# Kernel optimization log

Hardware: AMD Instinct MI355X
Metric: run time of the kernel (lower is better)

## Reference

```python
import jax, jax.numpy as jnp
import numpy as np

IN_CH, OUT_CH, IN_W, K, PAD = 64, 64, 2048, 3, 1
OUT_W = IN_W + 2 * PAD - K + 1  # 2048


def setup_inputs() -> dict:
    key = jax.random.key(0)
    k1, k2, k3 = jax.random.split(key, 3)
    x = jax.random.normal(k1, (32, IN_CH, IN_W), dtype=jnp.float32)
    weights = jax.random.normal(k2, (OUT_W, OUT_CH, IN_CH, K), dtype=jnp.float32)
    bias = jax.random.normal(k3, (OUT_CH, OUT_W), dtype=jnp.float32)
    return {"x": x, "weights": weights, "bias": bias}


def reference(x, weights, bias):
    # x: (B, IC, W); weights: (OW, OC, IC, K); bias: (OC, OW)
    xp = jnp.pad(x, ((0, 0), (0, 0), (PAD, PAD)))  # (B, IC, W+2p)
    # Gather sliding windows: patches[b, ic, w, k] = xp[b, ic, w + k]
    idx = jnp.arange(OUT_W)[:, None] + jnp.arange(K)[None, :]  # (OW, K)
    patches = xp[:, :, idx]  # (B, IC, OW, K)
    # Per-position unshared contraction over (ic, k)
    out = jnp.einsum('bcwk,wock->bow', patches, weights)  # (B, OC, OW)
    return out + bias[None, :, :]
```

## Files before the change

kernel.cpp:

```cpp
#include <hip/hip_runtime.h>
#include <hip/hip_bf16.h>

typedef _Float16 f16x4 __attribute__((ext_vector_type(4)));
typedef _Float16 f16x8 __attribute__((ext_vector_type(8)));
typedef float f32x4 __attribute__((ext_vector_type(4)));

#define IN_CH   64
#define OUT_CH  64
#define W_TOT   2048
#define KW      3
#define B_TOT   32
#define CK      192
#define LDSTRIDE 200

__global__ __launch_bounds__(256, 4)
void lc1d_kernel(const float* __restrict__ x,
                 const float* __restrict__ wts,
                 const float* __restrict__ bias,
                 float* __restrict__ out) {
    __shared__ _Float16 Wt[OUT_CH * LDSTRIDE];
    __shared__ _Float16 Xp[B_TOT * LDSTRIDE];

    const int tid = threadIdx.x;
    const int bid = blockIdx.x;
    const int w = (bid & 7) * 256 + (bid >> 3);

    const float* wsrc = wts + (size_t)w * (OUT_CH * CK);
    #pragma unroll
    for (int i = 0; i < 12; ++i) {
        int e = i * 1024 + tid * 4;
        float4 v = *reinterpret_cast<const float4*>(wsrc + e);
        int r = e / CK;
        int c = e - r * CK;
        f16x4 h = { (_Float16)v.x, (_Float16)v.y, (_Float16)v.z, (_Float16)v.w };
        *reinterpret_cast<f16x4*>(&Wt[r * LDSTRIDE + c]) = h;
    }

    #pragma unroll
    for (int j = 0; j < 8; ++j) {
        int p = tid + 256 * j;
        int b = p >> 6;
        int c = p & 63;
        const float* row = x + (size_t)p * W_TOT;
        #pragma unroll
        for (int k = 0; k < KW; ++k) {
            int v = w - 1 + k;
            float xv = (v >= 0 && v < W_TOT) ? row[v] : 0.0f;
            Xp[b * LDSTRIDE + c * 3 + k] = (_Float16)xv;
        }
    }

    __syncthreads();

    const int lane = tid & 63;
    const int wv   = tid >> 6;
    const int l15  = lane & 15;
    const int kg   = lane >> 4;

    const _Float16* Xb = &Xp[l15 * LDSTRIDE + kg * 8];
    const _Float16* Wb = &Wt[(wv * 16 + l15) * LDSTRIDE + kg * 8];

    f32x4 acc0 = {0.f, 0.f, 0.f, 0.f};
    f32x4 acc1 = {0.f, 0.f, 0.f, 0.f};
    #pragma unroll
    for (int kk = 0; kk < 6; ++kk) {
        f16x8 a0 = *reinterpret_cast<const f16x8*>(Xb + kk * 32);
        f16x8 a1 = *reinterpret_cast<const f16x8*>(Xb + 16 * LDSTRIDE + kk * 32);
        f16x8 bf = *reinterpret_cast<const f16x8*>(Wb + kk * 32);
        acc0 = __builtin_amdgcn_mfma_f32_16x16x32_f16(a0, bf, acc0, 0, 0, 0);
        acc1 = __builtin_amdgcn_mfma_f32_16x16x32_f16(a1, bf, acc1, 0, 0, 0);
    }

    const int o = wv * 16 + l15;
    const float bv = bias[o * W_TOT + w];
    #pragma unroll
    for (int r = 0; r < 4; ++r) {
        int b0 = kg * 4 + r;
        out[((size_t)(b0 * OUT_CH + o)) * W_TOT + w] = acc0[r] + bv;
        int b1 = 16 + kg * 4 + r;
        out[((size_t)(b1 * OUT_CH + o)) * W_TOT + w] = acc1[r] + bv;
    }
}

extern "C" void kernel_launch(void* const* d_in, const int* in_sizes, int n_in,
                              void* d_out, int out_size, void* d_ws, size_t ws_size,
                              hipStream_t stream) {
    const float* x    = (const float*)d_in[0];
    const float* wts  = (const float*)d_in[1];
    const float* bias = (const float*)d_in[2];
    float* out = (float*)d_out;
    hipLaunchKernelGGL(lc1d_kernel, dim3(2048), dim3(256), 0, stream,
                       x, wts, bias, out);
}
```

Baseline: 219.3 us.

## Load weight fragments directly into registers and batch x window loads

Weights are now read from global memory straight into the per-lane MFMA B-fragment registers, dropping the shared-memory weight tile and its round trip. The x window loads are issued as float2 vector loads into registers before any LDS stores, so all global loads are in flight together. Removing the weight tile shrinks LDS use, and the occupancy hint goes from 4 to 5 blocks. In exchange, each lane's global weight reads are 32-byte chunks at a 768-byte stride rather than fully coalesced float4 rows, and register pressure rises.

```diff
diff --git a/kernel.cpp b/kernel.cpp
--- a/kernel.cpp
+++ b/kernel.cpp
@@ -1,7 +1,5 @@
 #include <hip/hip_runtime.h>
-#include <hip/hip_bf16.h>
 
-typedef _Float16 f16x4 __attribute__((ext_vector_type(4)));
 typedef _Float16 f16x8 __attribute__((ext_vector_type(8)));
 typedef float f32x4 __attribute__((ext_vector_type(4)));
 
@@ -11,68 +9,91 @@
 #define KW      3
 #define B_TOT   32
 #define CK      192
-#define LDSTRIDE 200
+#define LDST    200
 
-__global__ __launch_bounds__(256, 4)
+static __device__ __forceinline__ f16x8 cvt8(const float4& a, const float4& b) {
+    f16x8 r;
+    r[0] = (_Float16)a.x; r[1] = (_Float16)a.y; r[2] = (_Float16)a.z; r[3] = (_Float16)a.w;
+    r[4] = (_Float16)b.x; r[5] = (_Float16)b.y; r[6] = (_Float16)b.z; r[7] = (_Float16)b.w;
+    return r;
+}
+
+__global__ __launch_bounds__(256, 5)
 void lc1d_kernel(const float* __restrict__ x,
                  const float* __restrict__ wts,
                  const float* __restrict__ bias,
                  float* __restrict__ out) {
-    __shared__ _Float16 Wt[OUT_CH * LDSTRIDE];
-    __shared__ _Float16 Xp[B_TOT * LDSTRIDE];
+    __shared__ _Float16 Xp[B_TOT * LDST];
 
     const int tid = threadIdx.x;
     const int bid = blockIdx.x;
     const int w = (bid & 7) * 256 + (bid >> 3);
 
-    const float* wsrc = wts + (size_t)w * (OUT_CH * CK);
+    const int lane = tid & 63;
+    const int wv   = tid >> 6;
+    const int l15  = lane & 15;
+    const int kg   = lane >> 4;
+
+    float xv[8][3];
     #pragma unroll
-    for (int i = 0; i < 12; ++i) {
-        int e = i * 1024 + tid * 4;
-        float4 v = *reinterpret_cast<const float4*>(wsrc + e);
-        int r = e / CK;
-        int c = e - r * CK;
-        f16x4 h = { (_Float16)v.x, (_Float16)v.y, (_Float16)v.z, (_Float16)v.w };
-        *reinterpret_cast<f16x4*>(&Wt[r * LDSTRIDE + c]) = h;
+    for (int j = 0; j < 8; ++j) {
+        const float* row = x + (size_t)(tid + 256 * j) * W_TOT;
+        if (w == 0) {
+            float2 lo = *reinterpret_cast<const float2*>(row);
+            xv[j][0] = 0.f;  xv[j][1] = lo.x; xv[j][2] = lo.y;
+        } else if (w == W_TOT - 1) {
+            float2 lo = *reinterpret_cast<const float2*>(row + W_TOT - 2);
+            xv[j][0] = lo.x; xv[j][1] = lo.y; xv[j][2] = 0.f;
+        } else if ((w - 1) & 1) {
+            float2 lo = *reinterpret_cast<const float2*>(row + (w - 1 - 1));
+            float2 hi = *reinterpret_cast<const float2*>(row + (w - 1 + 1));
+            xv[j][0] = lo.y; xv[j][1] = hi.x; xv[j][2] = hi.y;
+        } else {
+            float2 lo = *reinterpret_cast<const float2*>(row + (w - 1));
+            float2 hi = *reinterpret_cast<const float2*>(row + (w + 1));
+            xv[j][0] = lo.x; xv[j][1] = lo.y; xv[j][2] = hi.x;
+        }
     }
+
+    const int o = wv * 16 + l15;
+    const float* wsrc = wts + (size_t)w * (OUT_CH * CK) + o * CK + kg * 8;
+    float4 wf[6][2];
+    #pragma unroll
+    for (int ks = 0; ks < 6; ++ks) {
+        wf[ks][0] = *reinterpret_cast<const float4*>(wsrc + ks * 32);
+        wf[ks][1] = *reinterpret_cast<const float4*>(wsrc + ks * 32 + 4);
+    }
+
+    const float bv = bias[o * W_TOT + w];
 
     #pragma unroll
     for (int j = 0; j < 8; ++j) {
         int p = tid + 256 * j;
         int b = p >> 6;
         int c = p & 63;
-        const float* row = x + (size_t)p * W_TOT;
-        #pragma unroll
-        for (int k = 0; k < KW; ++k) {
-            int v = w - 1 + k;
-            float xv = (v >= 0 && v < W_TOT) ? row[v] : 0.0f;
-            Xp[b * LDSTRIDE + c * 3 + k] = (_Float16)xv;
-        }
+        _Float16* dst = &Xp[b * LDST + c * 3];
+        dst[0] = (_Float16)xv[j][0];
+        dst[1] = (_Float16)xv[j][1];
+        dst[2] = (_Float16)xv[j][2];
     }
+
+    f16x8 bw[6];
+    #pragma unroll
+    for (int ks = 0; ks < 6; ++ks) bw[ks] = cvt8(wf[ks][0], wf[ks][1]);
 
     __syncthreads();
 
-    const int lane = tid & 63;
-    const int wv   = tid >> 6;
-    const int l15  = lane & 15;
-    const int kg   = lane >> 4;
-
-    const _Float16* Xb = &Xp[l15 * LDSTRIDE + kg * 8];
-    const _Float16* Wb = &Wt[(wv * 16 + l15) * LDSTRIDE + kg * 8];
-
+    const _Float16* Xb = &Xp[l15 * LDST + kg * 8];
     f32x4 acc0 = {0.f, 0.f, 0.f, 0.f};
     f32x4 acc1 = {0.f, 0.f, 0.f, 0.f};
     #pragma unroll
-    for (int kk = 0; kk < 6; ++kk) {
-        f16x8 a0 = *reinterpret_cast<const f16x8*>(Xb + kk * 32);
-        f16x8 a1 = *reinterpret_cast<const f16x8*>(Xb + 16 * LDSTRIDE + kk * 32);
-        f16x8 bf = *reinterpret_cast<const f16x8*>(Wb + kk * 32);
-        acc0 = __builtin_amdgcn_mfma_f32_16x16x32_f16(a0, bf, acc0, 0, 0, 0);
-        acc1 = __builtin_amdgcn_mfma_f32_16x16x32_f16(a1, bf, acc1, 0, 0, 0);
+    for (int ks = 0; ks < 6; ++ks) {
+        f16x8 a0 = *reinterpret_cast<const f16x8*>(Xb + ks * 32);
+        f16x8 a1 = *reinterpret_cast<const f16x8*>(Xb + 16 * LDST + ks * 32);
+        acc0 = __builtin_amdgcn_mfma_f32_16x16x32_f16(a0, bw[ks], acc0, 0, 0, 0);
+        acc1 = __builtin_amdgcn_mfma_f32_16x16x32_f16(a1, bw[ks], acc1, 0, 0, 0);
     }
 
-    const int o = wv * 16 + l15;
-    const float bv = bias[o * W_TOT + w];
     #pragma unroll
     for (int r = 0; r < 4; ++r) {
         int b0 = kg * 4 + r;
```

New measurement: 207.7 us. 5.3% less time.

## Process four output positions per block with double-buffered weight prefetch

Applied to the files above, without the earlier changes.

Each block now handles four consecutive output positions instead of one. Weights for the next position are prefetched into registers and written into a double-buffered LDS tile while the current position's MFMAs run. The input window is loaded once as six contiguous values per row instead of three scattered scalar loads per position. Outputs and bias are written and read as float4 vectors. This cuts redundant x loads, uncoalesced stores and per-block setup. In exchange there are four times fewer blocks, more registers per thread and extra barriers.

```diff
diff --git a/kernel.cpp b/kernel.cpp
--- a/kernel.cpp
+++ b/kernel.cpp
@@ -1,85 +1,144 @@
 #include <hip/hip_runtime.h>
-#include <hip/hip_bf16.h>
+#include <stdint.h>
 
-typedef _Float16 f16x4 __attribute__((ext_vector_type(4)));
 typedef _Float16 f16x8 __attribute__((ext_vector_type(8)));
+typedef _Float16 f16x4v __attribute__((ext_vector_type(4)));
 typedef float f32x4 __attribute__((ext_vector_type(4)));
 
-#define IN_CH   64
-#define OUT_CH  64
-#define W_TOT   2048
-#define KW      3
-#define B_TOT   32
-#define CK      192
-#define LDSTRIDE 200
+#define W_TOT  2048
+#define CK     192
+#define NW     4
+#define WROWST 200
+#define XPST   200
 
-__global__ __launch_bounds__(256, 4)
+__global__ __launch_bounds__(256, 2)
 void lc1d_kernel(const float* __restrict__ x,
                  const float* __restrict__ wts,
                  const float* __restrict__ bias,
                  float* __restrict__ out) {
-    __shared__ _Float16 Wt[OUT_CH * LDSTRIDE];
-    __shared__ _Float16 Xp[B_TOT * LDSTRIDE];
+    __shared__ _Float16 Wb[2][64 * WROWST];
+    __shared__ _Float16 Xp[32 * XPST];
 
-    const int tid = threadIdx.x;
-    const int bid = blockIdx.x;
-    const int w = (bid & 7) * 256 + (bid >> 3);
-
-    const float* wsrc = wts + (size_t)w * (OUT_CH * CK);
-    #pragma unroll
-    for (int i = 0; i < 12; ++i) {
-        int e = i * 1024 + tid * 4;
-        float4 v = *reinterpret_cast<const float4*>(wsrc + e);
-        int r = e / CK;
-        int c = e - r * CK;
-        f16x4 h = { (_Float16)v.x, (_Float16)v.y, (_Float16)v.z, (_Float16)v.w };
-        *reinterpret_cast<f16x4*>(&Wt[r * LDSTRIDE + c]) = h;
-    }
-
-    #pragma unroll
-    for (int j = 0; j < 8; ++j) {
-        int p = tid + 256 * j;
-        int b = p >> 6;
-        int c = p & 63;
-        const float* row = x + (size_t)p * W_TOT;
-        #pragma unroll
-        for (int k = 0; k < KW; ++k) {
-            int v = w - 1 + k;
-            float xv = (v >= 0 && v < W_TOT) ? row[v] : 0.0f;
-            Xp[b * LDSTRIDE + c * 3 + k] = (_Float16)xv;
-        }
-    }
-
-    __syncthreads();
+    const int tid  = threadIdx.x;
+    const int bid  = blockIdx.x;
+    const int w0   = ((bid & 7) * 64 + (bid >> 3)) * NW;
 
     const int lane = tid & 63;
     const int wv   = tid >> 6;
     const int l15  = lane & 15;
     const int kg   = lane >> 4;
+    const int o    = wv * 16 + l15;
 
-    const _Float16* Xb = &Xp[l15 * LDSTRIDE + kg * 8];
-    const _Float16* Wb = &Wt[(wv * 16 + l15) * LDSTRIDE + kg * 8];
-
-    f32x4 acc0 = {0.f, 0.f, 0.f, 0.f};
-    f32x4 acc1 = {0.f, 0.f, 0.f, 0.f};
+    float xw[8][6];
     #pragma unroll
-    for (int kk = 0; kk < 6; ++kk) {
-        f16x8 a0 = *reinterpret_cast<const f16x8*>(Xb + kk * 32);
-        f16x8 a1 = *reinterpret_cast<const f16x8*>(Xb + 16 * LDSTRIDE + kk * 32);
-        f16x8 bf = *reinterpret_cast<const f16x8*>(Wb + kk * 32);
-        acc0 = __builtin_amdgcn_mfma_f32_16x16x32_f16(a0, bf, acc0, 0, 0, 0);
-        acc1 = __builtin_amdgcn_mfma_f32_16x16x32_f16(a1, bf, acc1, 0, 0, 0);
+    for (int j = 0; j < 8; ++j) {
+        const float* row = x + (size_t)(tid + 256 * j) * W_TOT;
+        if (w0 == 0) {
+            float2 a = *(const float2*)(row + 0);
+            float2 b = *(const float2*)(row + 2);
+            float2 c = *(const float2*)(row + 4);
+            xw[j][0] = 0.f;  xw[j][1] = a.x; xw[j][2] = a.y;
+            xw[j][3] = b.x;  xw[j][4] = b.y; xw[j][5] = c.x;
+        } else if (w0 == W_TOT - NW) {
+            float2 a = *(const float2*)(row + W_TOT - 6);
+            float2 b = *(const float2*)(row + W_TOT - 4);
+            float2 c = *(const float2*)(row + W_TOT - 2);
+            xw[j][0] = a.y; xw[j][1] = b.x; xw[j][2] = b.y;
+            xw[j][3] = c.x; xw[j][4] = c.y; xw[j][5] = 0.f;
+        } else {
+            float2 a = *(const float2*)(row + w0 - 2);
+            float2 b = *(const float2*)(row + w0);
+            float2 c = *(const float2*)(row + w0 + 2);
+            float2 d = *(const float2*)(row + w0 + 4);
+            xw[j][0] = a.y; xw[j][1] = b.x; xw[j][2] = b.y;
+            xw[j][3] = c.x; xw[j][4] = c.y; xw[j][5] = d.x;
+        }
     }
 
-    const int o = wv * 16 + l15;
-    const float bv = bias[o * W_TOT + w];
+    f32x4 wr[12];
+    {
+        const float* wp = wts + (size_t)w0 * (64 * CK);
+        #pragma unroll
+        for (int t = 0; t < 12; ++t)
+            wr[t] = *(const f32x4*)(wp + t * 1024 + tid * 4);
+    }
+    const f32x4 bv = *(const f32x4*)(bias + (size_t)o * W_TOT + w0);
+
+    _Float16 xh[8][6];
     #pragma unroll
-    for (int r = 0; r < 4; ++r) {
-        int b0 = kg * 4 + r;
-        out[((size_t)(b0 * OUT_CH + o)) * W_TOT + w] = acc0[r] + bv;
-        int b1 = 16 + kg * 4 + r;
-        out[((size_t)(b1 * OUT_CH + o)) * W_TOT + w] = acc1[r] + bv;
+    for (int j = 0; j < 8; ++j)
+        #pragma unroll
+        for (int s = 0; s < 6; ++s) xh[j][s] = (_Float16)xw[j][s];
+
+    #pragma unroll
+    for (int t = 0; t < 12; ++t) {
+        int e = t * 1024 + tid * 4;
+        int r = e / 192, c = e % 192;
+        f16x4v h = { (_Float16)wr[t][0], (_Float16)wr[t][1],
+                     (_Float16)wr[t][2], (_Float16)wr[t][3] };
+        *(f16x4v*)(&Wb[0][r * WROWST + c]) = h;
     }
+    #pragma unroll
+    for (int j = 0; j < 8; ++j) {
+        int p = tid + 256 * j;
+        _Float16* dst = &Xp[(p >> 6) * XPST + (p & 63) * 3];
+        dst[0] = xh[j][0]; dst[1] = xh[j][1]; dst[2] = xh[j][2];
+    }
+    __syncthreads();
+
+    f32x4 acc[NW][2];
+    #pragma unroll
+    for (int i = 0; i < NW; ++i) { acc[i][0] = {0.f,0.f,0.f,0.f}; acc[i][1] = {0.f,0.f,0.f,0.f}; }
+
+    const _Float16* Xb = &Xp[l15 * XPST + kg * 8];
+
+    #pragma unroll
+    for (int i = 0; i < NW; ++i) {
+        if (i < NW - 1) {
+            const float* wp = wts + (size_t)(w0 + i + 1) * (64 * CK);
+            #pragma unroll
+            for (int t = 0; t < 12; ++t)
+                wr[t] = *(const f32x4*)(wp + t * 1024 + tid * 4);
+        }
+        const _Float16* Wcur = &Wb[i & 1][o * WROWST + kg * 8];
+        #pragma unroll
+        for (int ks = 0; ks < 6; ++ks) {
+            f16x8 a0 = *(const f16x8*)(Xb + ks * 32);
+            f16x8 a1 = *(const f16x8*)(Xb + 16 * XPST + ks * 32);
+            f16x8 bw = *(const f16x8*)(Wcur + ks * 32);
+            acc[i][0] = __builtin_amdgcn_mfma_f32_16x16x32_f16(a0, bw, acc[i][0], 0, 0, 0);
+            acc[i][1] = __builtin_amdgcn_mfma_f32_16x16x32_f16(a1, bw, acc[i][1], 0, 0, 0);
+        }
+        __syncthreads();
+        if (i < NW - 1) {
+            _Float16* Wnxt = &Wb[(i + 1) & 1][0];
+            #pragma unroll
+            for (int t = 0; t < 12; ++t) {
+                int e = t * 1024 + tid * 4;
+                int r = e / 192, c = e % 192;
+                f16x4v h = { (_Float16)wr[t][0], (_Float16)wr[t][1],
+                             (_Float16)wr[t][2], (_Float16)wr[t][3] };
+                *(f16x4v*)(&Wnxt[r * WROWST + c]) = h;
+            }
+            #pragma unroll
+            for (int j = 0; j < 8; ++j) {
+                int p = tid + 256 * j;
+                _Float16* dst = &Xp[(p >> 6) * XPST + (p & 63) * 3];
+                dst[0] = xh[j][i + 1]; dst[1] = xh[j][i + 2]; dst[2] = xh[j][i + 3];
+            }
+            __syncthreads();
+        }
+    }
+
+    #pragma unroll
+    for (int bt = 0; bt < 2; ++bt)
+        #pragma unroll
+        for (int r = 0; r < 4; ++r) {
+            int b = bt * 16 + kg * 4 + r;
+            f32x4 v = { acc[0][bt][r] + bv[0], acc[1][bt][r] + bv[1],
+                        acc[2][bt][r] + bv[2], acc[3][bt][r] + bv[3] };
+            *(f32x4*)(out + ((size_t)(b * 64 + o)) * W_TOT + w0) = v;
+        }
 }
 
 extern "C" void kernel_launch(void* const* d_in, const int* in_sizes, int n_in,
@@ -89,6 +148,6 @@
     const float* wts  = (const float*)d_in[1];
     const float* bias = (const float*)d_in[2];
     float* out = (float*)d_out;
-    hipLaunchKernelGGL(lc1d_kernel, dim3(2048), dim3(256), 0, stream,
+    hipLaunchKernelGGL(lc1d_kernel, dim3(512), dim3(256), 0, stream,
                        x, wts, bias, out);
 }
```

Result: faster. 184.3 us (-15.9%).
